# Performance work log

Measured on AMD Instinct MI355X. Metric: run time of the kernel, lower is better.

The kernel has to match this reference:

```python
import jax, jax.numpy as jnp
import numpy as np

N = 50000      # nodes
E = 800000     # edges (before self-loops)
IN = 256       # input_dim
HID = 72       # hidden_dim
HEADS = 4
NEG_SLOPE = 0.2  # PyG GATConv default leaky-relu slope


def setup_inputs() -> dict:
    key = jax.random.key(0)
    ks = jax.random.split(key, 16)
    rn = lambda k, shape: jax.random.normal(k, shape, jnp.float32) * 0.05
    return {
        "x": jax.random.normal(ks[0], (N, IN), jnp.float32),
        "edge_index": jax.random.randint(ks[1], (2, E), 0, N),
        "W_in": rn(ks[2], (IN, HID)), "b_in": jnp.zeros((HID,), jnp.float32),
        "W1": rn(ks[3], (HID, HEADS * HID)),
        "a_src1": rn(ks[4], (HEADS, HID)), "a_dst1": rn(ks[5], (HEADS, HID)),
        "b1": jnp.zeros((HEADS * HID,), jnp.float32),
        "W2": rn(ks[6], (HEADS * HID, HID)),
        "a_src2": rn(ks[7], (1, HID)), "a_dst2": rn(ks[8], (1, HID)),
        "b2": jnp.zeros((HID,), jnp.float32),
        "W3": rn(ks[9], (HID, HID)),
        "a_src3": rn(ks[10], (1, HID)), "a_dst3": rn(ks[11], (1, HID)),
        "b3": jnp.zeros((HID,), jnp.float32),
        "Ws1": rn(ks[12], (HID, 32)), "bs1": jnp.zeros((32,), jnp.float32),
        "Ws2": rn(ks[13], (32, 1)), "bs2": jnp.zeros((1,), jnp.float32),
    }


def gat_conv(x, src, dst, W, a_src, a_dst, bias, concat):
    # PyG GATConv (eval mode): per-head linear, leaky-relu attention logits,
    # segment softmax over incoming edges per destination, scatter-aggregate.
    H, C = a_src.shape
    h = (x @ W).reshape(-1, H, C)                      # [N, H, C]
    logit_s = jnp.einsum('nhc,hc->nh', h, a_src)       # [N, H]
    logit_d = jnp.einsum('nhc,hc->nh', h, a_dst)       # [N, H]
    e = jax.nn.leaky_relu(logit_s[src] + logit_d[dst], NEG_SLOPE)   # [Et, H]
    emax = jax.ops.segment_max(e, dst, num_segments=N)
    emax = jnp.where(jnp.isfinite(emax), emax, 0.0)
    p = jnp.exp(e - emax[dst])
    denom = jax.ops.segment_sum(p, dst, num_segments=N)
    alpha = p / jnp.maximum(denom[dst], 1e-16)         # [Et, H]
    out = jax.ops.segment_sum(h[src] * alpha[:, :, None], dst, num_segments=N)
    out = out.reshape(-1, H * C) if concat else out.mean(axis=1)
    return out + bias


def reference(x, edge_index, W_in, b_in,
              W1, a_src1, a_dst1, b1,
              W2, a_src2, a_dst2, b2,
              W3, a_src3, a_dst3, b3,
              Ws1, bs1, Ws2, bs2):
    loops = jnp.arange(N)                              # PyG add_self_loops=True
    src = jnp.concatenate([edge_index[0], loops])
    dst = jnp.concatenate([edge_index[1], loops])
    x0 = x @ W_in + b_in                               # [N, HID]
    h = jax.nn.elu(gat_conv(x0, src, dst, W1, a_src1, a_dst1, b1, True))
    h = jax.nn.elu(gat_conv(h, src, dst, W2, a_src2, a_dst2, b2, False))
    h = jax.nn.elu(gat_conv(h, src, dst, W3, a_src3, a_dst3, b3, False))
    h = h + x0
    score = jax.nn.relu(h @ Ws1 + bs1) @ Ws2 + bs2     # dropout = identity (eval)
    return score.squeeze(-1)                           # [N]
```

## Files before the change

kernel.cpp:

```cpp
#include <hip/hip_runtime.h>
#include <hip/hip_fp16.h>
#include <cmath>

#define NN 50000
#define EE 800000
#define ET (EE + NN)
#define IN_DIM 256
#define HID 72
#define CAP 96

typedef __attribute__((ext_vector_type(8))) short s8v;
typedef __attribute__((ext_vector_type(4))) short s4v;
typedef __attribute__((ext_vector_type(4))) float f4v;
typedef __attribute__((ext_vector_type(2))) float f2v;

__device__ __forceinline__ ushort f2bf(float x) {
    uint u = __float_as_uint(x);
    return (ushort)((u + 0x7fffu + ((u >> 16) & 1u)) >> 16);
}
__device__ __forceinline__ float bf2f(ushort h) {
    return __uint_as_float(((uint)h) << 16);
}
__device__ __forceinline__ void split4(const float4& v, s4v& h, s4v& l) {
    ushort h0 = f2bf(v.x), h1 = f2bf(v.y), h2 = f2bf(v.z), h3 = f2bf(v.w);
    h = (s4v){(short)h0, (short)h1, (short)h2, (short)h3};
    l = (s4v){(short)f2bf(v.x - bf2f(h0)), (short)f2bf(v.y - bf2f(h1)),
              (short)f2bf(v.z - bf2f(h2)), (short)f2bf(v.w - bf2f(h3))};
}
__device__ __forceinline__ f4v mfma16(s8v a, s8v b, f4v c) {
    return __builtin_amdgcn_mfma_f32_16x16x32_bf16(a, b, c, 0, 0, 0);
}
__device__ __forceinline__ f2v unpack_h2(uint pv) {
    __half2 hv = __builtin_bit_cast(__half2, pv);
    return (f2v){__low2float(hv), __high2float(hv)};
}
__device__ __forceinline__ uint pack_h2(float a, float b) {
    __half2 hp = __floats2half2_rn(a, b);
    return __builtin_bit_cast(uint, hp);
}
__device__ __forceinline__ f2v fma2(float w, f2v c, f2v a) {
    return __builtin_elementwise_fma((f2v){w, w}, c, a);
}

__device__ __forceinline__ void wsplit_one(const float* W, int ldw, int K,
        int idx, short* outH, short* outL) {
    int h = idx / (72 * K);
    int rem = idx - h * 72 * K;
    int n = rem / K, k = rem - n * K;
    float v = W[(size_t)k * ldw + h * 72 + n];
    ushort hi = f2bf(v);
    outH[idx] = (short)hi;
    outL[idx] = (short)f2bf(v - bf2f(hi));
}

#define PR0 18432
#define PR1 (PR0 + 20736)
#define PR2 (PR1 + 20736)
#define PR3 (PR2 + 5184)
#define PRTOT (PR3 + 288)

__global__ __launch_bounds__(256) void prep_kernel(
        const float* __restrict__ W_in, const float* __restrict__ W1,
        const float* __restrict__ W2, const float* __restrict__ W3,
        const float* __restrict__ a_src, const float* __restrict__ a_dst,
        short* __restrict__ BtInH, short* __restrict__ BtInL,
        short* __restrict__ Bt1H, short* __restrict__ Bt1L,
        short* __restrict__ Bt2H, short* __restrict__ Bt2L,
        short* __restrict__ Bt3H, short* __restrict__ Bt3L,
        float* __restrict__ wsrc, float* __restrict__ wdst) {
    int gid = blockIdx.x * 256 + threadIdx.x;
    if (gid < PR0) {
        wsplit_one(W_in, 72, 256, gid, BtInH, BtInL);
    } else if (gid < PR1) {
        wsplit_one(W1, 288, 72, gid - PR0, Bt1H, Bt1L);
    } else if (gid < PR2) {
        wsplit_one(W2, 72, 288, gid - PR1, Bt2H, Bt2L);
    } else if (gid < PR3) {
        wsplit_one(W3, 72, 72, gid - PR2, Bt3H, Bt3L);
    } else if (gid < PRTOT) {
        int j = gid - PR3;
        int h = j / HID, k = j % HID;
        const float* wrow = W1 + (size_t)k * (4 * HID) + h * HID;
        const float* as = a_src + h * HID;
        const float* ad = a_dst + h * HID;
        float s = 0.f, d = 0.f;
        for (int c = 0; c < HID; ++c) {
            float w = wrow[c];
            s = fmaf(w, as[c], s);
            d = fmaf(w, ad[c], d);
        }
        wsrc[j] = s;
        wdst[j] = d;
    }
}

template <int NLOGIT, bool ELU_EPI, bool BATCHED, bool PACKOUT, bool APACK, bool ADJ>
__global__ __launch_bounds__(256) void gemm_mfma(
        const void* __restrict__ Ain, const short* __restrict__ BtH,
        const short* __restrict__ BtL, const float* __restrict__ bias,
        float* __restrict__ C, uint* __restrict__ Cp, int ldp,
        const float* __restrict__ lvs, const float* __restrict__ lvd,
        float* __restrict__ ls, float* __restrict__ ld,
        int M, int K, int lda, int Nfull,
        const int* __restrict__ eiw, int* __restrict__ degw,
        ushort* __restrict__ ellw, int gemmBlocks) {
    __shared__ __align__(16) short AhS[64 * 40], AlS[64 * 40];
    __shared__ __align__(16) short BhS[80 * 40], BlS[80 * 40];

    int tid = threadIdx.x;

    if (ADJ && (int)blockIdx.x >= gemmBlocks) {
        int t = (blockIdx.x - gemmBlocks) * 256 + tid;
        int i0 = t * 4;
        if (i0 < ET) {
            if (i0 + 3 < EE) {
                int4 s4 = *(const int4*)(eiw + i0);
                int4 d4 = *(const int4*)(eiw + EE + i0);
                int ss[4] = {s4.x, s4.y, s4.z, s4.w};
                int dd[4] = {d4.x, d4.y, d4.z, d4.w};
                #pragma unroll
                for (int u = 0; u < 4; ++u) {
                    int pos = atomicAdd(&degw[dd[u]], 1);
                    if (pos < CAP) ellw[dd[u] * CAP + pos] = (ushort)ss[u];
                }
            } else {
                #pragma unroll
                for (int u = 0; u < 4; ++u) {
                    int i = i0 + u;
                    if (i < ET) {
                        int src = (i < EE) ? eiw[i] : (i - EE);
                        int dst = (i < EE) ? eiw[EE + i] : (i - EE);
                        int pos = atomicAdd(&degw[dst], 1);
                        if (pos < CAP) ellw[dst * CAP + pos] = (ushort)src;
                    }
                }
            }
        }
        return;
    }

    int row0 = blockIdx.x * 64;
    int hh = BATCHED ? blockIdx.y : 0;
    int aoff = BATCHED ? hh * (APACK ? 36 : 72) : 0;
    int coff = BATCHED ? hh * 72 : 0;
    const short* bhg = BtH + (size_t)hh * 72 * K;
    const short* blg = BtL + (size_t)hh * 72 * K;

    for (int i = tid; i < 8 * 40; i += 256) {
        BhS[72 * 40 + i] = 0;
        BlS[72 * 40 + i] = 0;
    }

    int w = tid >> 6;
    int lane = tid & 63;
    int q = lane >> 4, l16 = lane & 15;

    f4v acc[5];
    #pragma unroll
    for (int f = 0; f < 5; ++f) acc[f] = (f4v)0.f;

    int ar = tid >> 2;
    int aseg = tid & 3;
    bool arok = (row0 + ar) < M;
    const float* aptrf = nullptr;
    const uint*  aptru = nullptr;
    if constexpr (APACK) {
        aptru = (const uint*)Ain + (size_t)(row0 + ar) * lda + aoff;
    } else {
        aptrf = (const float*)Ain + (size_t)(row0 + ar) * lda + aoff;
    }
    int bn0 = tid >> 2, bq0 = tid & 3;
    int bn1 = (tid + 256) >> 2;

    float4 va, vb;
    s8v bh0, bl0, bh1, bl1;
    auto gload = [&](int k0) {
        va = (float4){0, 0, 0, 0};
        vb = (float4){0, 0, 0, 0};
        int ka = k0 + aseg * 8;
        if constexpr (APACK) {
            if (arok && ka < K) {
                uint4 u = *(const uint4*)(aptru + (ka >> 1));
                f2v p0 = unpack_h2(u.x), p1 = unpack_h2(u.y);
                f2v p2 = unpack_h2(u.z), p3 = unpack_h2(u.w);
                va = (float4){p0.x, p0.y, p1.x, p1.y};
                vb = (float4){p2.x, p2.y, p3.x, p3.y};
            }
        } else {
            if (arok && ka < K)     va = *(const float4*)(aptrf + ka);
            if (arok && ka + 4 < K) vb = *(const float4*)(aptrf + ka + 4);
        }
        bh0 = (s8v)0; bl0 = (s8v)0;
        int kb = k0 + bq0 * 8;
        if (kb < K) {
            bh0 = *(const s8v*)(bhg + (size_t)bn0 * K + kb);
            bl0 = *(const s8v*)(blg + (size_t)bn0 * K + kb);
        }
        bh1 = (s8v)0; bl1 = (s8v)0;
        if (tid < 32 && kb < K) {
            bh1 = *(const s8v*)(bhg + (size_t)bn1 * K + kb);
            bl1 = *(const s8v*)(blg + (size_t)bn1 * K + kb);
        }
    };
    auto commit = [&]() {
        s4v h0, l0, h1, l1;
        split4(va, h0, l0);
        split4(vb, h1, l1);
        *(s4v*)&AhS[ar * 40 + aseg * 8]     = h0;
        *(s4v*)&AhS[ar * 40 + aseg * 8 + 4] = h1;
        *(s4v*)&AlS[ar * 40 + aseg * 8]     = l0;
        *(s4v*)&AlS[ar * 40 + aseg * 8 + 4] = l1;
        *(s8v*)&BhS[bn0 * 40 + bq0 * 8] = bh0;
        *(s8v*)&BlS[bn0 * 40 + bq0 * 8] = bl0;
        if (tid < 32) {
            *(s8v*)&BhS[bn1 * 40 + bq0 * 8] = bh1;
            *(s8v*)&BlS[bn1 * 40 + bq0 * 8] = bl1;
        }
    };

    int ntiles = (K + 31) / 32;
    gload(0);
    for (int t = 0; t < ntiles; ++t) {
        commit();
        __syncthreads();
        if (t + 1 < ntiles) gload((t + 1) * 32);
        s8v ah = *(const s8v*)&AhS[(w * 16 + l16) * 40 + q * 8];
        s8v al = *(const s8v*)&AlS[(w * 16 + l16) * 40 + q * 8];
        #pragma unroll
        for (int f = 0; f < 5; ++f) {
            s8v bh = *(const s8v*)&BhS[(f * 16 + l16) * 40 + q * 8];
            s8v bl = *(const s8v*)&BlS[(f * 16 + l16) * 40 + q * 8];
            acc[f] = mfma16(ah, bh, acc[f]);
            acc[f] = mfma16(ah, bl, acc[f]);
            acc[f] = mfma16(al, bh, acc[f]);
        }
        __syncthreads();
    }

    float v[5][4];
    #pragma unroll
    for (int f = 0; f < 5; ++f) {
        int col = f * 16 + l16;
        bool cv = col < 72;
        #pragma unroll
        for (int r = 0; r < 4; ++r) {
            float t = acc[f][r];
            if (cv && bias) t += bias[coff + col];
            if (ELU_EPI) t = (t > 0.f) ? t : expm1f(t);
            v[f][r] = cv ? t : 0.f;
        }
    }
    if (NLOGIT > 0) {
        #pragma unroll
        for (int h2 = 0; h2 < NLOGIT; ++h2) {
            #pragma unroll
            for (int r = 0; r < 4; ++r) {
                float s = 0.f, d = 0.f;
                #pragma unroll
                for (int f = 0; f < 5; ++f) {
                    int col = f * 16 + l16;
                    float lw = (col < 72) ? lvs[h2 * 72 + col] : 0.f;
                    float dw = (col < 72) ? lvd[h2 * 72 + col] : 0.f;
                    s = fmaf(v[f][r], lw, s);
                    d = fmaf(v[f][r], dw, d);
                }
                s += __shfl_xor(s, 1); s += __shfl_xor(s, 2);
                s += __shfl_xor(s, 4); s += __shfl_xor(s, 8);
                d += __shfl_xor(d, 1); d += __shfl_xor(d, 2);
                d += __shfl_xor(d, 4); d += __shfl_xor(d, 8);
                int gr = row0 + w * 16 + q * 4 + r;
                if (l16 == 0 && gr < M) {
                    ls[gr * NLOGIT + h2] = s;
                    ld[gr * NLOGIT + h2] = d;
                }
            }
        }
    }
    if (PACKOUT) {
        #pragma unroll
        for (int f = 0; f < 5; ++f) {
            int col = f * 16 + l16;
            #pragma unroll
            for (int r = 0; r < 4; ++r) {
                float vo = __shfl_xor(v[f][r], 1);
                if ((l16 & 1) == 0 && col < 72) {
                    int gr = row0 + w * 16 + q * 4 + r;
                    if (gr < M) {
                        Cp[(size_t)gr * ldp + ((coff + col) >> 1)] =
                            pack_h2(v[f][r], vo);
                    }
                }
            }
        }
    }
    if (C != nullptr) {
        #pragma unroll
        for (int f = 0; f < 5; ++f) {
            int col = f * 16 + l16;
            if (col >= 72) continue;
            #pragma unroll
            for (int r = 0; r < 4; ++r) {
                int gr = row0 + w * 16 + q * 4 + r;
                if (gr < M) C[(size_t)gr * Nfull + coff + col] = v[f][r];
            }
        }
    }
}

template <int H, bool EPI, bool ADD_RES, bool POUT>
__global__ __launch_bounds__(64) void agg_gather(
        const uint* __restrict__ featp,
        const float* __restrict__ ls, const float* __restrict__ ld,
        const int* __restrict__ degv, const ushort* __restrict__ ell,
        const float* __restrict__ bias, const float* __restrict__ res,
        float* __restrict__ out, uint* __restrict__ outp, int n) {
    __shared__ float wsh[64 * H];
    __shared__ int ssh[64];
    int wid = blockIdx.x;
    int lane = threadIdx.x;
    int deg = min(degv[wid], CAP);
    const ushort* row = ell + (size_t)wid * CAP;

    float ldh[H];
    if (H == 4) {
        float4 t = ((const float4*)ld)[wid];
        ldh[0] = t.x; ldh[1] = t.y; ldh[2] = t.z; ldh[3] = t.w;
    } else {
        ldh[0] = ld[wid];
    }

    f2v acc2[H];
    #pragma unroll
    for (int h = 0; h < H; ++h) acc2[h] = (f2v)0.f;

    if (deg <= 64) {
        bool act = lane < deg;
        int s = row[act ? lane : 0];
        ssh[lane] = s;
        float e[H];
        float ev[H];
        if (H == 4) {
            float4 lv = ((const float4*)ls)[s];
            ev[0] = lv.x; ev[1] = lv.y; ev[2] = lv.z; ev[3] = lv.w;
        } else {
            ev[0] = ls[s];
        }
        #pragma unroll
        for (int h = 0; h < H; ++h) {
            float vv = ev[h] + ldh[h];
            vv = (vv > 0.f) ? vv : 0.2f * vv;
            e[h] = act ? vv : -__builtin_inff();
        }
        float wv[H];
        #pragma unroll
        for (int h = 0; h < H; ++h) {
            float mh = e[h];
            #pragma unroll
            for (int off = 32; off; off >>= 1) mh = fmaxf(mh, __shfl_xor(mh, off));
            float ph = act ? expf(e[h] - mh) : 0.f;
            float sh = ph;
            #pragma unroll
            for (int off = 32; off; off >>= 1) sh += __shfl_xor(sh, off);
            wv[h] = ph / fmaxf(sh, 1e-16f);
        }
        if (H == 4) {
            ((float4*)wsh)[lane] = (float4){wv[0], wv[1], wv[2], wv[3]};
        } else {
            wsh[lane] = wv[0];
        }
        __syncthreads();

        int nb = (deg + 7) & ~7;
        const uint* rowbase = featp + (lane < 36 ? lane : 0);
        for (int t = 0; t < nb; t += 8) {
            int si[8];
            #pragma unroll
            for (int u = 0; u < 8; ++u) si[u] = ssh[t + u];
            uint pv[8];
            #pragma unroll
            for (int u = 0; u < 8; ++u) pv[u] = rowbase[(size_t)si[u] * 36];
            #pragma unroll
            for (int u = 0; u < 8; ++u) {
                f2v c2 = unpack_h2(pv[u]);
                if constexpr (H == 4) {
                    float4 we = ((const float4*)wsh)[t + u];
                    acc2[0] = fma2(we.x, c2, acc2[0]);
                    acc2[1] = fma2(we.y, c2, acc2[1]);
                    acc2[2] = fma2(we.z, c2, acc2[2]);
                    acc2[3] = fma2(we.w, c2, acc2[3]);
                } else {
                    acc2[0] = fma2(wsh[t + u], c2, acc2[0]);
                }
            }
        }
    } else {
        float m[H];
        #pragma unroll
        for (int h = 0; h < H; ++h) m[h] = -__builtin_inff();
        for (int i = lane; i < deg; i += 64) {
            int s = row[i];
            float e[H];
            if (H == 4) {
                float4 lv = ((const float4*)ls)[s];
                e[0] = lv.x; e[1] = lv.y; e[2] = lv.z; e[3] = lv.w;
            } else {
                e[0] = ls[s];
            }
            #pragma unroll
            for (int h = 0; h < H; ++h) {
                float vv = e[h] + ldh[h];
                vv = (vv > 0.f) ? vv : 0.2f * vv;
                m[h] = fmaxf(m[h], vv);
            }
        }
        #pragma unroll
        for (int h = 0; h < H; ++h)
            #pragma unroll
            for (int off = 32; off; off >>= 1) m[h] = fmaxf(m[h], __shfl_xor(m[h], off));

        float ssum[H];
        #pragma unroll
        for (int h = 0; h < H; ++h) ssum[h] = 0.f;
        for (int i = lane; i < deg; i += 64) {
            int s = row[i];
            float e[H];
            if (H == 4) {
                float4 lv = ((const float4*)ls)[s];
                e[0] = lv.x; e[1] = lv.y; e[2] = lv.z; e[3] = lv.w;
            } else {
                e[0] = ls[s];
            }
            #pragma unroll
            for (int h = 0; h < H; ++h) {
                float vv = e[h] + ldh[h];
                vv = (vv > 0.f) ? vv : 0.2f * vv;
                ssum[h] += expf(vv - m[h]);
            }
        }
        #pragma unroll
        for (int h = 0; h < H; ++h)
            #pragma unroll
            for (int off = 32; off; off >>= 1) ssum[h] += __shfl_xor(ssum[h], off);
        float inv[H];
        #pragma unroll
        for (int h = 0; h < H; ++h) inv[h] = 1.f / fmaxf(ssum[h], 1e-16f);

        for (int base = 0; base < deg; base += 64) {
            int i = base + lane;
            int lim = min(64, deg - base);
            if (i < deg) {
                int s = row[i];
                ssh[lane] = s;
                float e[H];
                if (H == 4) {
                    float4 lv = ((const float4*)ls)[s];
                    e[0] = lv.x; e[1] = lv.y; e[2] = lv.z; e[3] = lv.w;
                } else {
                    e[0] = ls[s];
                }
                if (H == 4) {
                    float p0 = expf(((e[0] + ldh[0] > 0.f) ? e[0] + ldh[0] : 0.2f * (e[0] + ldh[0])) - m[0]) * inv[0];
                    float p1 = expf(((e[1] + ldh[1] > 0.f) ? e[1] + ldh[1] : 0.2f * (e[1] + ldh[1])) - m[1]) * inv[1];
                    float p2 = expf(((e[2] + ldh[2] > 0.f) ? e[2] + ldh[2] : 0.2f * (e[2] + ldh[2])) - m[2]) * inv[2];
                    float p3 = expf(((e[3] + ldh[3] > 0.f) ? e[3] + ldh[3] : 0.2f * (e[3] + ldh[3])) - m[3]) * inv[3];
                    ((float4*)wsh)[lane] = (float4){p0, p1, p2, p3};
                } else {
                    float vv = e[0] + ldh[0];
                    vv = (vv > 0.f) ? vv : 0.2f * vv;
                    wsh[lane] = expf(vv - m[0]) * inv[0];
                }
            }
            __syncthreads();
            for (int t = 0; t < lim; ++t) {
                uint pv = featp[(size_t)ssh[t] * 36 + (lane < 36 ? lane : 0)];
                f2v c2 = unpack_h2(pv);
                if constexpr (H == 4) {
                    float4 we = ((const float4*)wsh)[t];
                    acc2[0] = fma2(we.x, c2, acc2[0]);
                    acc2[1] = fma2(we.y, c2, acc2[1]);
                    acc2[2] = fma2(we.z, c2, acc2[2]);
                    acc2[3] = fma2(we.w, c2, acc2[3]);
                } else {
                    acc2[0] = fma2(wsh[t], c2, acc2[0]);
                }
            }
            __syncthreads();
        }
    }

    if (lane < 36) {
        #pragma unroll
        for (int h = 0; h < H; ++h) {
            float v0 = acc2[h].x, v1 = acc2[h].y;
            if (EPI) {
                v0 += bias[2 * lane];
                v1 += bias[2 * lane + 1];
                v0 = (v0 > 0.f) ? v0 : expm1f(v0);
                v1 = (v1 > 0.f) ? v1 : expm1f(v1);
                if (ADD_RES) {
                    float2 rr = *(const float2*)&res[(size_t)wid * HID + 2 * lane];
                    v0 += rr.x; v1 += rr.y;
                }
            }
            if (POUT) {
                outp[(size_t)wid * (H * 36) + h * 36 + lane] = pack_h2(v0, v1);
            } else {
                *(float2*)&out[(size_t)wid * (H * HID) + h * HID + 2 * lane] =
                    (float2){v0, v1};
            }
        }
    }
}

__global__ __launch_bounds__(256) void score_kernel(
        const float* __restrict__ h, const float* __restrict__ Ws1, const float* __restrict__ bs1,
        const float* __restrict__ Ws2, const float* __restrict__ bs2,
        float* __restrict__ out, int n) {
    int sub = threadIdx.x >> 5;
    int j = threadIdx.x & 31;
    int node = blockIdx.x * 8 + sub;
    if (node >= n) return;
    const float* row = h + (size_t)node * HID;
    float acc = bs1[j];
    #pragma unroll 8
    for (int c = 0; c < HID; ++c) acc = fmaf(row[c], Ws1[c * 32 + j], acc);
    float v = fmaxf(acc, 0.f) * Ws2[j];
    #pragma unroll
    for (int off = 16; off; off >>= 1) v += __shfl_down(v, off, 32);
    if (j == 0) out[node] = v + bs2[0];
}

extern "C" void kernel_launch(void* const* d_in, const int* in_sizes, int n_in,
                              void* d_out, int out_size, void* d_ws, size_t ws_size,
                              hipStream_t stream) {
    const float* x      = (const float*)d_in[0];
    const int*   ei     = (const int*)  d_in[1];
    const float* W_in   = (const float*)d_in[2];
    const float* b_in   = (const float*)d_in[3];
    const float* W1     = (const float*)d_in[4];
    const float* a_src1 = (const float*)d_in[5];
    const float* a_dst1 = (const float*)d_in[6];
    const float* b1     = (const float*)d_in[7];
    const float* W2     = (const float*)d_in[8];
    const float* a_src2 = (const float*)d_in[9];
    const float* a_dst2 = (const float*)d_in[10];
    const float* b2     = (const float*)d_in[11];
    const float* W3     = (const float*)d_in[12];
    const float* a_src3 = (const float*)d_in[13];
    const float* a_dst3 = (const float*)d_in[14];
    const float* b3     = (const float*)d_in[15];
    const float* Ws1    = (const float*)d_in[16];
    const float* bs1    = (const float*)d_in[17];
    const float* Ws2    = (const float*)d_in[18];
    const float* bs2    = (const float*)d_in[19];
    float* out = (float*)d_out;

    float* ws    = (float*)d_ws;
    float* x0    = ws;
    float* h3    = x0 + (size_t)NN * HID;
    float* ls    = h3 + (size_t)NN * HID;
    float* ld    = ls + (size_t)NN * 4;
    float* wsrc1 = ld + (size_t)NN * 4;
    float* wdst1 = wsrc1 + 288;
    int* deg     = (int*)(wdst1 + 288);
    ushort* ell  = (ushort*)(deg + NN);
    uintptr_t bp = ((uintptr_t)(ell + (size_t)NN * CAP) + 15) & ~(uintptr_t)15;
    short* BtInH = (short*)bp;
    short* BtInL = BtInH + 18432;
    short* Bt1H  = BtInL + 18432;
    short* Bt1L  = Bt1H + 20736;
    short* Bt2H  = Bt1L + 20736;
    short* Bt2L  = Bt2H + 20736;
    short* Bt3H  = Bt2L + 20736;
    short* Bt3L  = Bt3H + 5184;
    uint*  x0p   = (uint*)(Bt3L + 5184);
    uint*  a1p   = x0p + (size_t)NN * 36;
    uint*  h1p   = a1p + (size_t)NN * 144;
    uint*  hp2p  = h1p + (size_t)NN * 144;
    uint*  h2p   = hp2p + (size_t)NN * 36;
    uint*  hp3p  = h2p + (size_t)NN * 36;

    hipMemsetAsync(deg, 0, NN * sizeof(int), stream);

    prep_kernel<<<(PRTOT + 255) / 256, 256, 0, stream>>>(
        W_in, W1, W2, W3, a_src1, a_dst1,
        BtInH, BtInL, Bt1H, Bt1L, Bt2H, Bt2L, Bt3H, Bt3L, wsrc1, wdst1);

    const int mblocks = (NN + 63) / 64;
    const int adjBlocks = (ET / 4 + 255) / 256;
    gemm_mfma<4, false, false, true, false, true>
        <<<dim3(mblocks + adjBlocks, 1), 256, 0, stream>>>(
        x, BtInH, BtInL, b_in, x0, x0p, 36, wsrc1, wdst1, ls, ld,
        NN, IN_DIM, IN_DIM, HID, ei, deg, ell, mblocks);
    agg_gather<4, false, false, true><<<NN, 64, 0, stream>>>(
        x0p, ls, ld, deg, ell, nullptr, nullptr, nullptr, a1p, NN);
    gemm_mfma<0, true, true, true, true, false><<<dim3(mblocks, 4), 256, 0, stream>>>(
        a1p, Bt1H, Bt1L, b1, nullptr, h1p, 144, nullptr, nullptr, nullptr, nullptr,
        NN, HID, 144, 0, nullptr, nullptr, nullptr, 0);
    gemm_mfma<1, false, false, true, true, false><<<dim3(mblocks, 1), 256, 0, stream>>>(
        h1p, Bt2H, Bt2L, nullptr, nullptr, hp2p, 36, a_src2, a_dst2, ls, ld,
        NN, 288, 144, 0, nullptr, nullptr, nullptr, 0);
    agg_gather<1, true, false, true><<<NN, 64, 0, stream>>>(
        hp2p, ls, ld, deg, ell, b2, nullptr, nullptr, h2p, NN);
    gemm_mfma<1, false, false, true, true, false><<<dim3(mblocks, 1), 256, 0, stream>>>(
        h2p, Bt3H, Bt3L, nullptr, nullptr, hp3p, 36, a_src3, a_dst3, ls, ld,
        NN, HID, 36, 0, nullptr, nullptr, nullptr, 0);
    agg_gather<1, true, true, false><<<NN, 64, 0, stream>>>(
        hp3p, ls, ld, deg, ell, b3, x0, h3, nullptr, NN);
    score_kernel<<<(NN + 7) / 8, 256, 0, stream>>>(h3, Ws1, bs1, Ws2, bs2, out, NN);
}
```

Before: 372.7 us.

## Partition adjacency build by destination range and initialize self-loops in prep

The ELL adjacency build now assigns each block a slice of 8192 edges and one of eight destination-node ranges. A block only does the atomicAdd and ELL write for edges whose destination falls in its range, so scattered atomics and writes stay inside a smaller region of memory. Self-loops and degree initialization move into prep_kernel (deg=1, first ELL slot = self), which removes the separate memset and the tail handling for self-loop edges. The cost is that every edge index is read eight times, once per range, across many more adjacency blocks.

```diff
diff --git a/kernel.cpp b/kernel.cpp
--- a/kernel.cpp
+++ b/kernel.cpp
@@ -8,6 +8,9 @@
 #define IN_DIM 256
 #define HID 72
 #define CAP 96
+#define NRANGE 8
+#define RSPAN (NN / NRANGE)
+#define SLICE_E 8192
 
 typedef __attribute__((ext_vector_type(8))) short s8v;
 typedef __attribute__((ext_vector_type(4))) short s4v;
@@ -57,7 +60,8 @@
 #define PR1 (PR0 + 20736)
 #define PR2 (PR1 + 20736)
 #define PR3 (PR2 + 5184)
-#define PRTOT (PR3 + 288)
+#define PR4 (PR3 + 288)
+#define PRTOT (PR4 + NN)
 
 __global__ __launch_bounds__(256) void prep_kernel(
         const float* __restrict__ W_in, const float* __restrict__ W1,
@@ -67,7 +71,8 @@
         short* __restrict__ Bt1H, short* __restrict__ Bt1L,
         short* __restrict__ Bt2H, short* __restrict__ Bt2L,
         short* __restrict__ Bt3H, short* __restrict__ Bt3L,
-        float* __restrict__ wsrc, float* __restrict__ wdst) {
+        float* __restrict__ wsrc, float* __restrict__ wdst,
+        int* __restrict__ deg, ushort* __restrict__ ell) {
     int gid = blockIdx.x * 256 + threadIdx.x;
     if (gid < PR0) {
         wsplit_one(W_in, 72, 256, gid, BtInH, BtInL);
@@ -77,7 +82,7 @@
         wsplit_one(W2, 72, 288, gid - PR1, Bt2H, Bt2L);
     } else if (gid < PR3) {
         wsplit_one(W3, 72, 72, gid - PR2, Bt3H, Bt3L);
-    } else if (gid < PRTOT) {
+    } else if (gid < PR4) {
         int j = gid - PR3;
         int h = j / HID, k = j % HID;
         const float* wrow = W1 + (size_t)k * (4 * HID) + h * HID;
@@ -91,6 +96,10 @@
         }
         wsrc[j] = s;
         wdst[j] = d;
+    } else if (gid < PRTOT) {
+        int i = gid - PR4;
+        deg[i] = 1;
+        ell[(size_t)i * CAP] = (ushort)i;
     }
 }
 
@@ -110,29 +119,24 @@
     int tid = threadIdx.x;
 
     if (ADJ && (int)blockIdx.x >= gemmBlocks) {
-        int t = (blockIdx.x - gemmBlocks) * 256 + tid;
-        int i0 = t * 4;
-        if (i0 < ET) {
-            if (i0 + 3 < EE) {
-                int4 s4 = *(const int4*)(eiw + i0);
-                int4 d4 = *(const int4*)(eiw + EE + i0);
-                int ss[4] = {s4.x, s4.y, s4.z, s4.w};
-                int dd[4] = {d4.x, d4.y, d4.z, d4.w};
-                #pragma unroll
-                for (int u = 0; u < 4; ++u) {
+        int ab = blockIdx.x - gemmBlocks;
+        int slice = ab >> 3;
+        int range = blockIdx.x & 7;
+        int lo = range * RSPAN;
+        int hi = lo + RSPAN;
+        #pragma unroll 2
+        for (int j = 0; j < 8; ++j) {
+            int i0 = slice * SLICE_E + j * 1024 + tid * 4;
+            if (i0 >= EE) break;
+            int4 d4 = *(const int4*)(eiw + EE + i0);
+            int4 s4 = *(const int4*)(eiw + i0);
+            int dd[4] = {d4.x, d4.y, d4.z, d4.w};
+            int ss[4] = {s4.x, s4.y, s4.z, s4.w};
+            #pragma unroll
+            for (int u = 0; u < 4; ++u) {
+                if (dd[u] >= lo && dd[u] < hi) {
                     int pos = atomicAdd(&degw[dd[u]], 1);
-                    if (pos < CAP) ellw[dd[u] * CAP + pos] = (ushort)ss[u];
-                }
-            } else {
-                #pragma unroll
-                for (int u = 0; u < 4; ++u) {
-                    int i = i0 + u;
-                    if (i < ET) {
-                        int src = (i < EE) ? eiw[i] : (i - EE);
-                        int dst = (i < EE) ? eiw[EE + i] : (i - EE);
-                        int pos = atomicAdd(&degw[dst], 1);
-                        if (pos < CAP) ellw[dst * CAP + pos] = (ushort)src;
-                    }
+                    if (pos < CAP) ellw[(size_t)dd[u] * CAP + pos] = (ushort)ss[u];
                 }
             }
         }
@@ -580,14 +584,14 @@
     uint*  h2p   = hp2p + (size_t)NN * 36;
     uint*  hp3p  = h2p + (size_t)NN * 36;
 
-    hipMemsetAsync(deg, 0, NN * sizeof(int), stream);
-
     prep_kernel<<<(PRTOT + 255) / 256, 256, 0, stream>>>(
         W_in, W1, W2, W3, a_src1, a_dst1,
-        BtInH, BtInL, Bt1H, Bt1L, Bt2H, Bt2L, Bt3H, Bt3L, wsrc1, wdst1);
+        BtInH, BtInL, Bt1H, Bt1L, Bt2H, Bt2L, Bt3H, Bt3L, wsrc1, wdst1,
+        deg, ell);
 
     const int mblocks = (NN + 63) / 64;
-    const int adjBlocks = (ET / 4 + 255) / 256;
+    const int nslice = (EE + SLICE_E - 1) / SLICE_E;
+    const int adjBlocks = nslice * NRANGE;
     gemm_mfma<4, false, false, true, false, true>
         <<<dim3(mblocks + adjBlocks, 1), 256, 0, stream>>>(
         x, BtInH, BtInL, b_in, x0, x0p, 36, wsrc1, wdst1, ls, ld,
```

Result: no change. 372.9 us (+0.0%).
